# Kernel optimization log

Measured on AMD Instinct MI355X. Metric: run time of the kernel, lower is better.

The kernel has to match this reference:

```python
import jax, jax.numpy as jnp
import numpy as np

N, F, B, D = 1500000, 64, 256, 64
S = B * D

def _lin(x, w, b):
    return x @ w + b

def setup_inputs() -> dict:
    key = jax.random.key(0)
    ks = jax.random.split(key, 32)
    def w(k, i, o):
        return jax.random.normal(k, (i, o), dtype=jnp.float32) * (1.0 / np.sqrt(i))
    inp = {
        "x": jax.random.normal(ks[0], (N, F), dtype=jnp.float32),
        "segment_ids": jnp.sort(jax.random.randint(ks[1], (N,), 0, S)),
        "B": B, "D": D,
        # table_forward (used inside no_grad kernel_forward)
        "tfc0_w": w(ks[2], F, 128), "tfc0_b": jnp.zeros((128,), jnp.float32),
        "tfc1_w": w(ks[3], 128, 32), "tfc1_b": jnp.zeros((32,), jnp.float32),
        # three kernel heads
        "fwd0_w": w(ks[4], 32, 64), "fwd0_b": jnp.zeros((64,), jnp.float32),
        "fwd1_w": w(ks[5], 64, 1), "fwd1_b": jnp.zeros((1,), jnp.float32),
        "com0_w": w(ks[6], 32, 64), "com0_b": jnp.zeros((64,), jnp.float32),
        "com1_w": w(ks[7], 64, 1), "com1_b": jnp.zeros((1,), jnp.float32),
        "bwd0_w": w(ks[8], 32, 64), "bwd0_b": jnp.zeros((64,), jnp.float32),
        "bwd1_w": w(ks[9], 64, 1), "bwd1_b": jnp.zeros((1,), jnp.float32),
        # rl table stack
        "rl0_w": w(ks[10], F, 128), "rl0_b": jnp.zeros((128,), jnp.float32),
        "rl1_w": w(ks[11], 128, 32), "rl1_b": jnp.zeros((32,), jnp.float32),
        # cost MLP
        "cost0_w": w(ks[12], 3, 64), "cost0_b": jnp.zeros((64,), jnp.float32),
        "cost1_w": w(ks[13], 64, 32), "cost1_b": jnp.zeros((32,), jnp.float32),
        # policy net
        "pol_w": w(ks[14], 64, 1), "pol_b": jnp.zeros((1,), jnp.float32),
    }
    return inp

def reference(x, segment_ids, B, D,
              tfc0_w, tfc0_b, tfc1_w, tfc1_b,
              fwd0_w, fwd0_b, fwd1_w, fwd1_b,
              com0_w, com0_b, com1_w, com1_b,
              bwd0_w, bwd0_b, bwd1_w, bwd1_b,
              rl0_w, rl0_b, rl1_w, rl1_b,
              cost0_w, cost0_b, cost1_w, cost1_b,
              pol_w, pol_b):
    S_ = B * D
    # kernel_forward (run under torch.no_grad in original)
    h = jax.nn.relu(_lin(x, tfc0_w, tfc0_b))        # [N,128]
    h = jax.nn.relu(_lin(h, tfc1_w, tfc1_b))        # [N,32]
    seg = jax.ops.segment_sum(h, segment_ids, num_segments=S_)  # [S,32]
    def head(w0, b0, w1, b1):
        return _lin(jax.nn.relu(_lin(seg, w0, b0)), w1, b1).ravel()  # [S]
    fwd_c = head(fwd0_w, fwd0_b, fwd1_w, fwd1_b)
    com_c = head(com0_w, com0_b, com1_w, com1_b)
    bwd_c = head(bwd0_w, bwd0_b, bwd1_w, bwd1_b)
    # _get_latent concatenates in kernel_forward return order (fwd, comm, bwd)
    cost_obs = jax.lax.stop_gradient(
        jnp.stack([fwd_c, com_c, bwd_c], axis=-1)).reshape(B, D, 3)
    c = jax.nn.relu(_lin(cost_obs, cost0_w, cost0_b))
    c = jax.nn.relu(_lin(c, cost1_w, cost1_b))       # [B,D,32]
    # rl table branch (differentiable)
    r = jax.nn.relu(_lin(x, rl0_w, rl0_b))
    r = jax.nn.relu(_lin(r, rl1_w, rl1_b))           # [N,32]
    r = jax.ops.segment_sum(r, segment_ids, num_segments=S_).reshape(B, D, 32)
    latent = jnp.concatenate([r, c], axis=-1)        # [B,D,64]
    logits = _lin(latent, pol_w, pol_b).squeeze(-1)  # [B,D]
    return logits
```

## Files before the change

kernel.cpp:

```cpp
#include <hip/hip_runtime.h>

typedef unsigned short u16;
typedef unsigned long long u64;
typedef __bf16  bf16x8 __attribute__((ext_vector_type(8)));
typedef float   f32x4  __attribute__((ext_vector_type(4)));

#define N_ROWS 1500000
#define S_SEG  16384
#define ROWS_PB 32
#define TILES_PB 15
#define GRID_MAIN 3125

#define XS_LD  72
#define H1B_LD 264

__device__ __forceinline__ u16 f2bf(float f) {
    union { __bf16 h; u16 u; } cv;
    cv.h = (__bf16)f;
    return cv.u;
}

__device__ __forceinline__ void barrier_nodrain() {
    asm volatile("s_waitcnt lgkmcnt(0)" ::: "memory");
    __builtin_amdgcn_s_barrier();
}

__global__ void zero_ws_kernel(float* p, int n4) {
    int i = blockIdx.x * 256 + threadIdx.x;
    if (i < n4) reinterpret_cast<float4*>(p)[i] = make_float4(0.f, 0.f, 0.f, 0.f);
}

__global__ void transpose_weights(const float* __restrict__ w0, const float* __restrict__ w1,
                                  const float* __restrict__ r0, const float* __restrict__ r1,
                                  u16* __restrict__ w0T, u16* __restrict__ w1T,
                                  u16* __restrict__ r0T, u16* __restrict__ r1T) {
    int idx = blockIdx.x * 256 + threadIdx.x;
    if (idx < 8192) {
        int o = idx >> 6, k = idx & 63;
        w0T[o * 64 + k] = f2bf(w0[k * 128 + o]);
    } else if (idx < 12288) {
        int t = idx - 8192; int o = t >> 7, k = t & 127;
        w1T[o * 128 + k] = f2bf(w1[k * 32 + o]);
    } else if (idx < 20480) {
        int t = idx - 12288; int o = t >> 6, k = t & 63;
        r0T[o * 64 + k] = f2bf(r0[k * 128 + o]);
    } else if (idx < 24576) {
        int t = idx - 20480; int o = t >> 7, k = t & 127;
        r1T[o * 128 + k] = f2bf(r1[k * 32 + o]);
    }
}

__global__ __launch_bounds__(512, 4) void main_mlp_seg(
    const float* __restrict__ x, const int* __restrict__ seg_ids,
    const u16* __restrict__ w0T, const float* __restrict__ b0a,
    const u16* __restrict__ w1T, const float* __restrict__ b1a,
    const u16* __restrict__ r0T, const float* __restrict__ rb0,
    const u16* __restrict__ r1T, const float* __restrict__ rb1,
    float* __restrict__ seg_out, float* __restrict__ rseg_out)
{
    __shared__ u16   xs [2][ROWS_PB * XS_LD];
    __shared__ u16   h1s[ROWS_PB * H1B_LD];
    __shared__ int   s_ids[2][ROWS_PB];
    __shared__ float bls0[256];
    __shared__ float bls1[64];

    const int tid = threadIdx.x;
    const int wid = tid >> 6, lane = tid & 63;
    const int m = lane & 15, q = lane >> 4;
    const size_t row0 = (size_t)blockIdx.x * (TILES_PB * ROWS_PB);

    const int brA = wid >> 2;
    const u16* W0 = brA ? r0T : w0T;
    const int brw = wid >> 2, rtw = (wid >> 1) & 1, ctw = wid & 1;
    const u16* W1 = brw ? r1T : w1T;

    bf16x8 wA[2][2];
    #pragma unroll
    for (int c = 0; c < 2; ++c) {
        int n0 = ((wid & 3) * 2 + c) * 16;
        wA[c][0] = *reinterpret_cast<const bf16x8*>(W0 + (n0 + m) * 64 + q * 8);
        wA[c][1] = *reinterpret_cast<const bf16x8*>(W0 + (n0 + m) * 64 + 32 + q * 8);
    }
    bf16x8 wB[4];
    #pragma unroll
    for (int ks = 0; ks < 4; ++ks)
        wB[ks] = *reinterpret_cast<const bf16x8*>(W1 + (ctw * 16 + m) * 128 + ks * 32 + q * 8);

    if (tid < 128)      bls0[tid] = b0a[tid];
    else if (tid < 256) bls0[tid] = rb0[tid - 128];
    else if (tid < 288) bls1[tid - 256] = b1a[tid - 256];
    else if (tid < 320) bls1[tid - 256] = rb1[tid - 288];

    const int sr = tid >> 4, sc4 = tid & 15;
    const float* xb = x + (row0 + sr) * 64 + sc4 * 4;
    const int xw = sr * XS_LD + sc4 * 4;

    {
        float4 v = *reinterpret_cast<const float4*>(xb);
        ushort4 pk;
        pk.x = f2bf(v.x); pk.y = f2bf(v.y); pk.z = f2bf(v.z); pk.w = f2bf(v.w);
        *reinterpret_cast<ushort4*>(&xs[0][xw]) = pk;
        if (tid < ROWS_PB) s_ids[0][tid] = seg_ids[row0 + tid];
    }
    float4 xr = *reinterpret_cast<const float4*>(xb + 2048);
    int idr = (tid < ROWS_PB) ? seg_ids[row0 + ROWS_PB + tid] : 0;
    barrier_nodrain();

    int   pid = -1;
    float pacc = 0.f;
    bool  have = false;
    float* __restrict__ sp = brw ? rseg_out : seg_out;
    const int colg = ctw * 16 + m;

    int cur = 0;
    #pragma unroll 1
    for (int t = 0; t < TILES_PB; ++t) {
        const int nxt = cur ^ 1;
        if (t + 1 < TILES_PB) {
            ushort4 pk;
            pk.x = f2bf(xr.x); pk.y = f2bf(xr.y); pk.z = f2bf(xr.z); pk.w = f2bf(xr.w);
            *reinterpret_cast<ushort4*>(&xs[nxt][xw]) = pk;
            if (tid < ROWS_PB) s_ids[nxt][tid] = idr;
        }
        if (t + 2 < TILES_PB) {
            xr = *reinterpret_cast<const float4*>(xb + (size_t)(t + 2) * 2048);
            if (tid < ROWS_PB) idr = seg_ids[row0 + (size_t)(t + 2) * ROWS_PB + tid];
        }
        #pragma unroll
        for (int rt = 0; rt < 2; ++rt) {
            bf16x8 a0 = *reinterpret_cast<const bf16x8*>(&xs[cur][(rt * 16 + m) * XS_LD + q * 8]);
            bf16x8 a1 = *reinterpret_cast<const bf16x8*>(&xs[cur][(rt * 16 + m) * XS_LD + 32 + q * 8]);
            #pragma unroll
            for (int c = 0; c < 2; ++c) {
                int n0 = ((wid & 3) * 2 + c) * 16;
                f32x4 acc = *reinterpret_cast<const f32x4*>(&bls0[brA * 128 + n0 + q * 4]);
                acc = __builtin_amdgcn_mfma_f32_16x16x32_bf16(wA[c][0], a0, acc, 0, 0, 0);
                acc = __builtin_amdgcn_mfma_f32_16x16x32_bf16(wA[c][1], a1, acc, 0, 0, 0);
                ushort4 pk;
                pk.x = f2bf(fmaxf(acc[0], 0.f));
                pk.y = f2bf(fmaxf(acc[1], 0.f));
                pk.z = f2bf(fmaxf(acc[2], 0.f));
                pk.w = f2bf(fmaxf(acc[3], 0.f));
                *reinterpret_cast<ushort4*>(
                    &h1s[(rt * 16 + m) * H1B_LD + brA * 128 + n0 + q * 4]) = pk;
            }
        }
        barrier_nodrain();

        {
            const int* ids = s_ids[cur];
            int l31 = (lane < 32) ? lane : 0;
            int ida = ids[l31];
            int idb = ids[l31 ? l31 - 1 : 0];
            u64 bmask = __ballot(lane > 0 && lane < 32 && ida != idb);

            bf16x8 a[4];
            #pragma unroll
            for (int ks = 0; ks < 4; ++ks)
                a[ks] = *reinterpret_cast<const bf16x8*>(
                    &h1s[(rtw * 16 + m) * H1B_LD + brw * 128 + ks * 32 + q * 8]);
            float bz = bls1[brw * 32 + colg];
            f32x4 acc = {bz, bz, bz, bz};
            #pragma unroll
            for (int ks = 0; ks < 4; ++ks)
                acc = __builtin_amdgcn_mfma_f32_16x16x32_bf16(a[ks], wB[ks], acc, 0, 0, 0);

            int start = 0;
            while (start < 32) {
                u64 above = bmask & (~0ull << (start + 1));
                int end = above ? (int)__builtin_ctzll(above) : 32;
                int sid = ids[start];
                if (sid != pid) {
                    if (have && q == 0) atomicAdd(&sp[pid * 32 + colg], pacc);
                    pid = sid; pacc = 0.f; have = false;
                }
                float s = 0.f;
                #pragma unroll
                for (int i = 0; i < 4; ++i) {
                    int row = rtw * 16 + q * 4 + i;
                    s += (row >= start && row < end) ? fmaxf(acc[i], 0.f) : 0.f;
                }
                s += __shfl_xor(s, 16);
                s += __shfl_xor(s, 32);
                if (end > rtw * 16 && start < rtw * 16 + 16) { pacc += s; have = true; }
                start = end;
            }
        }
        barrier_nodrain();
        cur = nxt;
    }
    if (have && q == 0) atomicAdd(&sp[pid * 32 + colg], pacc);
}

__global__ __launch_bounds__(256) void heads_kernel(
    const float* __restrict__ seg, const float* __restrict__ rseg,
    const float* __restrict__ fwd0_w, const float* __restrict__ fwd0_b,
    const float* __restrict__ fwd1_w, const float* __restrict__ fwd1_b,
    const float* __restrict__ com0_w, const float* __restrict__ com0_b,
    const float* __restrict__ com1_w, const float* __restrict__ com1_b,
    const float* __restrict__ bwd0_w, const float* __restrict__ bwd0_b,
    const float* __restrict__ bwd1_w, const float* __restrict__ bwd1_b,
    const float* __restrict__ cost0_w, const float* __restrict__ cost0_b,
    const float* __restrict__ cost1_w, const float* __restrict__ cost1_b,
    const float* __restrict__ pol_w, const float* __restrict__ pol_b,
    float* __restrict__ out)
{
    __shared__ float s_seg[4][32];
    __shared__ float s_rseg[4][32];
    __shared__ float s_c0[4][64];
    const int tid = threadIdx.x, wid = tid >> 6, lane = tid & 63;
    const int s = blockIdx.x * 4 + wid;

    if (lane < 32) {
        s_seg[wid][lane]  = seg[s * 32 + lane];
        s_rseg[wid][lane] = rseg[s * 32 + lane];
    }
    __syncthreads();

    const float* w0s[3] = {fwd0_w, com0_w, bwd0_w};
    const float* b0s[3] = {fwd0_b, com0_b, bwd0_b};
    const float* w1s[3] = {fwd1_w, com1_w, bwd1_w};
    const float* b1s[3] = {fwd1_b, com1_b, bwd1_b};
    float costs[3];
    #pragma unroll
    for (int hh = 0; hh < 3; ++hh) {
        float t = 0.f;
        #pragma unroll
        for (int k = 0; k < 32; ++k)
            t = fmaf(s_seg[wid][k], w0s[hh][k * 64 + lane], t);
        t = fmaxf(t + b0s[hh][lane], 0.f);
        float red = t * w1s[hh][lane];
        red += __shfl_down(red, 32);
        red += __shfl_down(red, 16);
        red += __shfl_down(red, 8);
        red += __shfl_down(red, 4);
        red += __shfl_down(red, 2);
        red += __shfl_down(red, 1);
        costs[hh] = __shfl(red, 0) + b1s[hh][0];
    }

    float c0 = costs[0] * cost0_w[lane] +
               costs[1] * cost0_w[64 + lane] +
               costs[2] * cost0_w[128 + lane] + cost0_b[lane];
    c0 = fmaxf(c0, 0.f);
    s_c0[wid][lane] = c0;
    __syncthreads();

    int kk = lane & 31;
    float c1 = 0.f;
    #pragma unroll 8
    for (int j = 0; j < 64; ++j)
        c1 = fmaf(s_c0[wid][j], cost1_w[j * 32 + kk], c1);
    c1 = fmaxf(c1 + cost1_b[kk], 0.f);

    float p = 0.f;
    if (lane < 32)
        p = s_rseg[wid][lane] * pol_w[lane] + c1 * pol_w[32 + lane];
    p += __shfl_down(p, 32);
    p += __shfl_down(p, 16);
    p += __shfl_down(p, 8);
    p += __shfl_down(p, 4);
    p += __shfl_down(p, 2);
    p += __shfl_down(p, 1);
    if (lane == 0) out[s] = p + pol_b[0];
}

extern "C" void kernel_launch(void* const* d_in, const int* in_sizes, int n_in,
                              void* d_out, int out_size, void* d_ws, size_t ws_size,
                              hipStream_t stream) {
    const float* x       = (const float*)d_in[0];
    const int*   seg_ids = (const int*)d_in[1];
    const float* tfc0_w = (const float*)d_in[4];
    const float* tfc0_b = (const float*)d_in[5];
    const float* tfc1_w = (const float*)d_in[6];
    const float* tfc1_b = (const float*)d_in[7];
    const float* fwd0_w = (const float*)d_in[8];
    const float* fwd0_b = (const float*)d_in[9];
    const float* fwd1_w = (const float*)d_in[10];
    const float* fwd1_b = (const float*)d_in[11];
    const float* com0_w = (const float*)d_in[12];
    const float* com0_b = (const float*)d_in[13];
    const float* com1_w = (const float*)d_in[14];
    const float* com1_b = (const float*)d_in[15];
    const float* bwd0_w = (const float*)d_in[16];
    const float* bwd0_b = (const float*)d_in[17];
    const float* bwd1_w = (const float*)d_in[18];
    const float* bwd1_b = (const float*)d_in[19];
    const float* rl0_w  = (const float*)d_in[20];
    const float* rl0_b  = (const float*)d_in[21];
    const float* rl1_w  = (const float*)d_in[22];
    const float* rl1_b  = (const float*)d_in[23];
    const float* cost0_w = (const float*)d_in[24];
    const float* cost0_b = (const float*)d_in[25];
    const float* cost1_w = (const float*)d_in[26];
    const float* cost1_b = (const float*)d_in[27];
    const float* pol_w   = (const float*)d_in[28];
    const float* pol_b   = (const float*)d_in[29];

    char* ws = (char*)d_ws;
    const size_t seg_bytes = (size_t)S_SEG * 32 * sizeof(float);
    float* seg  = (float*)ws;
    float* rseg = (float*)(ws + seg_bytes);
    u16* w0T = (u16*)(ws + 2 * seg_bytes);
    u16* w1T = w0T + 128 * 64;
    u16* r0T = w1T + 32 * 128;
    u16* r1T = r0T + 128 * 64;

    int n4 = (int)(2 * seg_bytes / 16);
    zero_ws_kernel<<<(n4 + 255) / 256, 256, 0, stream>>>(seg, n4);
    transpose_weights<<<96, 256, 0, stream>>>(tfc0_w, tfc1_w, rl0_w, rl1_w,
                                              w0T, w1T, r0T, r1T);
    main_mlp_seg<<<GRID_MAIN, 512, 0, stream>>>(
        x, seg_ids, w0T, tfc0_b, w1T, tfc1_b, r0T, rl0_b, r1T, rl1_b, seg, rseg);
    heads_kernel<<<S_SEG / 4, 256, 0, stream>>>(
        seg, rseg,
        fwd0_w, fwd0_b, fwd1_w, fwd1_b,
        com0_w, com0_b, com1_w, com1_b,
        bwd0_w, bwd0_b, bwd1_w, bwd1_b,
        cost0_w, cost0_b, cost1_w, cost1_b,
        pol_w, pol_b, (float*)d_out);
}
```

Baseline: 627.3 us.

## Software-pipeline layer1/layer2 across tiles with double-buffered h1 and one barrier

The main kernel now double-buffers the hidden activation tile in shared memory. Layer 2 and the segment reduction for tile i-1 run in the same phase as layer 1 for tile i, which leaves one barrier per iteration instead of two. Biases are held in registers instead of shared memory, and the zeroing and weight-transpose kernels are merged into one launch. In exchange, shared memory use per block and register pressure both rise, which could lower occupancy.

```diff
diff --git a/kernel.cpp b/kernel.cpp
--- a/kernel.cpp
+++ b/kernel.cpp
@@ -25,16 +25,17 @@
     __builtin_amdgcn_s_barrier();
 }
 
-__global__ void zero_ws_kernel(float* p, int n4) {
-    int i = blockIdx.x * 256 + threadIdx.x;
-    if (i < n4) reinterpret_cast<float4*>(p)[i] = make_float4(0.f, 0.f, 0.f, 0.f);
-}
-
-__global__ void transpose_weights(const float* __restrict__ w0, const float* __restrict__ w1,
-                                  const float* __restrict__ r0, const float* __restrict__ r1,
-                                  u16* __restrict__ w0T, u16* __restrict__ w1T,
-                                  u16* __restrict__ r0T, u16* __restrict__ r1T) {
-    int idx = blockIdx.x * 256 + threadIdx.x;
+__global__ void prep_kernel(float* p, int n4,
+                            const float* __restrict__ w0, const float* __restrict__ w1,
+                            const float* __restrict__ r0, const float* __restrict__ r1,
+                            u16* __restrict__ w0T, u16* __restrict__ w1T,
+                            u16* __restrict__ r0T, u16* __restrict__ r1T) {
+    if (blockIdx.x < 1024) {
+        int i = blockIdx.x * 256 + threadIdx.x;
+        if (i < n4) reinterpret_cast<float4*>(p)[i] = make_float4(0.f, 0.f, 0.f, 0.f);
+        return;
+    }
+    int idx = (blockIdx.x - 1024) * 256 + threadIdx.x;
     if (idx < 8192) {
         int o = idx >> 6, k = idx & 63;
         w0T[o * 64 + k] = f2bf(w0[k * 128 + o]);
@@ -58,11 +59,9 @@
     const u16* __restrict__ r1T, const float* __restrict__ rb1,
     float* __restrict__ seg_out, float* __restrict__ rseg_out)
 {
-    __shared__ u16   xs [2][ROWS_PB * XS_LD];
-    __shared__ u16   h1s[ROWS_PB * H1B_LD];
-    __shared__ int   s_ids[2][ROWS_PB];
-    __shared__ float bls0[256];
-    __shared__ float bls1[64];
+    __shared__ u16 xs [2][ROWS_PB * XS_LD];
+    __shared__ u16 h1s[2][ROWS_PB * H1B_LD];
+    __shared__ int s_ids[4][ROWS_PB];
 
     const int tid = threadIdx.x;
     const int wid = tid >> 6, lane = tid & 63;
@@ -70,26 +69,27 @@
     const size_t row0 = (size_t)blockIdx.x * (TILES_PB * ROWS_PB);
 
     const int brA = wid >> 2;
-    const u16* W0 = brA ? r0T : w0T;
+    const u16*   W0  = brA ? r0T : w0T;
+    const float* B0g = brA ? rb0 : b0a;
     const int brw = wid >> 2, rtw = (wid >> 1) & 1, ctw = wid & 1;
-    const u16* W1 = brw ? r1T : w1T;
+    const u16*   W1  = brw ? r1T : w1T;
+    const float* B1g = brw ? rb1 : b1a;
 
     bf16x8 wA[2][2];
+    f32x4  b0v[2];
     #pragma unroll
     for (int c = 0; c < 2; ++c) {
         int n0 = ((wid & 3) * 2 + c) * 16;
         wA[c][0] = *reinterpret_cast<const bf16x8*>(W0 + (n0 + m) * 64 + q * 8);
         wA[c][1] = *reinterpret_cast<const bf16x8*>(W0 + (n0 + m) * 64 + 32 + q * 8);
+        b0v[c]   = *reinterpret_cast<const f32x4*>(B0g + n0 + q * 4);
     }
     bf16x8 wB[4];
     #pragma unroll
     for (int ks = 0; ks < 4; ++ks)
         wB[ks] = *reinterpret_cast<const bf16x8*>(W1 + (ctw * 16 + m) * 128 + ks * 32 + q * 8);
-
-    if (tid < 128)      bls0[tid] = b0a[tid];
-    else if (tid < 256) bls0[tid] = rb0[tid - 128];
-    else if (tid < 288) bls1[tid - 256] = b1a[tid - 256];
-    else if (tid < 320) bls1[tid - 256] = rb1[tid - 288];
+    const int colg = ctw * 16 + m;
+    const float bz = B1g[colg];
 
     const int sr = tid >> 4, sc4 = tid & 15;
     const float* xb = x + (row0 + sr) * 64 + sc4 * 4;
@@ -110,45 +110,46 @@
     float pacc = 0.f;
     bool  have = false;
     float* __restrict__ sp = brw ? rseg_out : seg_out;
-    const int colg = ctw * 16 + m;
-
-    int cur = 0;
+
     #pragma unroll 1
-    for (int t = 0; t < TILES_PB; ++t) {
-        const int nxt = cur ^ 1;
-        if (t + 1 < TILES_PB) {
-            ushort4 pk;
-            pk.x = f2bf(xr.x); pk.y = f2bf(xr.y); pk.z = f2bf(xr.z); pk.w = f2bf(xr.w);
-            *reinterpret_cast<ushort4*>(&xs[nxt][xw]) = pk;
-            if (tid < ROWS_PB) s_ids[nxt][tid] = idr;
-        }
-        if (t + 2 < TILES_PB) {
-            xr = *reinterpret_cast<const float4*>(xb + (size_t)(t + 2) * 2048);
-            if (tid < ROWS_PB) idr = seg_ids[row0 + (size_t)(t + 2) * ROWS_PB + tid];
-        }
-        #pragma unroll
-        for (int rt = 0; rt < 2; ++rt) {
-            bf16x8 a0 = *reinterpret_cast<const bf16x8*>(&xs[cur][(rt * 16 + m) * XS_LD + q * 8]);
-            bf16x8 a1 = *reinterpret_cast<const bf16x8*>(&xs[cur][(rt * 16 + m) * XS_LD + 32 + q * 8]);
+    for (int i = 0; i <= TILES_PB; ++i) {
+        if (i < TILES_PB) {
+            if (i + 1 < TILES_PB) {
+                ushort4 pk;
+                pk.x = f2bf(xr.x); pk.y = f2bf(xr.y); pk.z = f2bf(xr.z); pk.w = f2bf(xr.w);
+                *reinterpret_cast<ushort4*>(&xs[(i + 1) & 1][xw]) = pk;
+                if (tid < ROWS_PB) s_ids[(i + 1) & 3][tid] = idr;
+            }
+            if (i + 2 < TILES_PB) {
+                xr = *reinterpret_cast<const float4*>(xb + (size_t)(i + 2) * 2048);
+                if (tid < ROWS_PB) idr = seg_ids[row0 + (size_t)(i + 2) * ROWS_PB + tid];
+            }
+            const u16* xsc = xs[i & 1];
+            u16* h1d = h1s[i & 1];
             #pragma unroll
-            for (int c = 0; c < 2; ++c) {
-                int n0 = ((wid & 3) * 2 + c) * 16;
-                f32x4 acc = *reinterpret_cast<const f32x4*>(&bls0[brA * 128 + n0 + q * 4]);
-                acc = __builtin_amdgcn_mfma_f32_16x16x32_bf16(wA[c][0], a0, acc, 0, 0, 0);
-                acc = __builtin_amdgcn_mfma_f32_16x16x32_bf16(wA[c][1], a1, acc, 0, 0, 0);
-                ushort4 pk;
-                pk.x = f2bf(fmaxf(acc[0], 0.f));
-                pk.y = f2bf(fmaxf(acc[1], 0.f));
-                pk.z = f2bf(fmaxf(acc[2], 0.f));
-                pk.w = f2bf(fmaxf(acc[3], 0.f));
-                *reinterpret_cast<ushort4*>(
-                    &h1s[(rt * 16 + m) * H1B_LD + brA * 128 + n0 + q * 4]) = pk;
+            for (int rt = 0; rt < 2; ++rt) {
+                bf16x8 a0 = *reinterpret_cast<const bf16x8*>(&xsc[(rt * 16 + m) * XS_LD + q * 8]);
+                bf16x8 a1 = *reinterpret_cast<const bf16x8*>(&xsc[(rt * 16 + m) * XS_LD + 32 + q * 8]);
+                #pragma unroll
+                for (int c = 0; c < 2; ++c) {
+                    int n0 = ((wid & 3) * 2 + c) * 16;
+                    f32x4 acc = b0v[c];
+                    acc = __builtin_amdgcn_mfma_f32_16x16x32_bf16(wA[c][0], a0, acc, 0, 0, 0);
+                    acc = __builtin_amdgcn_mfma_f32_16x16x32_bf16(wA[c][1], a1, acc, 0, 0, 0);
+                    ushort4 pk;
+                    pk.x = f2bf(fmaxf(acc[0], 0.f));
+                    pk.y = f2bf(fmaxf(acc[1], 0.f));
+                    pk.z = f2bf(fmaxf(acc[2], 0.f));
+                    pk.w = f2bf(fmaxf(acc[3], 0.f));
+                    *reinterpret_cast<ushort4*>(
+                        &h1d[(rt * 16 + m) * H1B_LD + brA * 128 + n0 + q * 4]) = pk;
+                }
             }
         }
-        barrier_nodrain();
-
-        {
-            const int* ids = s_ids[cur];
+        if (i > 0) {
+            const int pt = i - 1;
+            const int* ids = s_ids[pt & 3];
+            const u16* h1c = h1s[pt & 1];
             int l31 = (lane < 32) ? lane : 0;
             int ida = ids[l31];
             int idb = ids[l31 ? l31 - 1 : 0];
@@ -158,8 +159,7 @@
             #pragma unroll
             for (int ks = 0; ks < 4; ++ks)
                 a[ks] = *reinterpret_cast<const bf16x8*>(
-                    &h1s[(rtw * 16 + m) * H1B_LD + brw * 128 + ks * 32 + q * 8]);
-            float bz = bls1[brw * 32 + colg];
+                    &h1c[(rtw * 16 + m) * H1B_LD + brw * 128 + ks * 32 + q * 8]);
             f32x4 acc = {bz, bz, bz, bz};
             #pragma unroll
             for (int ks = 0; ks < 4; ++ks)
@@ -176,9 +176,9 @@
                 }
                 float s = 0.f;
                 #pragma unroll
-                for (int i = 0; i < 4; ++i) {
-                    int row = rtw * 16 + q * 4 + i;
-                    s += (row >= start && row < end) ? fmaxf(acc[i], 0.f) : 0.f;
+                for (int ii = 0; ii < 4; ++ii) {
+                    int row = rtw * 16 + q * 4 + ii;
+                    s += (row >= start && row < end) ? fmaxf(acc[ii], 0.f) : 0.f;
                 }
                 s += __shfl_xor(s, 16);
                 s += __shfl_xor(s, 32);
@@ -186,8 +186,7 @@
                 start = end;
             }
         }
-        barrier_nodrain();
-        cur = nxt;
+        if (i < TILES_PB) barrier_nodrain();
     }
     if (have && q == 0) atomicAdd(&sp[pid * 32 + colg], pacc);
 }
@@ -307,9 +306,9 @@
     u16* r1T = r0T + 128 * 64;
 
     int n4 = (int)(2 * seg_bytes / 16);
-    zero_ws_kernel<<<(n4 + 255) / 256, 256, 0, stream>>>(seg, n4);
-    transpose_weights<<<96, 256, 0, stream>>>(tfc0_w, tfc1_w, rl0_w, rl1_w,
-                                              w0T, w1T, r0T, r1T);
+    prep_kernel<<<1024 + 96, 256, 0, stream>>>(seg, n4,
+                                               tfc0_w, tfc1_w, rl0_w, rl1_w,
+                                               w0T, w1T, r0T, r1T);
     main_mlp_seg<<<GRID_MAIN, 512, 0, stream>>>(
         x, seg_ids, w0T, tfc0_b, w1T, tfc1_b, r0T, rl0_b, r1T, rl1_b, seg, rseg);
     heads_kernel<<<S_SEG / 4, 256, 0, stream>>>(
```

Result: no change. 619.3 us (-1.3%).
